# Kernel optimization log

Measured on AMD Instinct MI355X. Metric: run time of the kernel, lower is better.

Reference implementation:

```python
import jax, jax.numpy as jnp
import numpy as np

B, S, D = 16, 16, 4096
H, KV, HD = 32, 8, 128
MAX_B, MAX_S = 16, 4096
START = 4080


def setup_inputs() -> dict:
    key = jax.random.key(0)
    ks = jax.random.split(key, 10)
    sc = 0.02
    # RoPE angles for positions [START, START+S)
    inv_freq = 1.0 / (10000.0 ** (np.arange(0, HD, 2, dtype=np.float32) / HD))  # [HD/2]
    pos = np.arange(START, START + S, dtype=np.float32)
    ang = np.outer(pos, inv_freq)  # [S, HD/2]
    return {
        'x': jax.random.normal(ks[0], (B, S, D), jnp.float32),
        'k': jax.random.normal(ks[1], (B, S, D), jnp.float32),
        'v': jax.random.normal(ks[2], (B, S, D), jnp.float32),
        'wq': jax.random.normal(ks[3], (D, H * HD), jnp.float32) * sc,
        'wk': jax.random.normal(ks[4], (D, KV * HD), jnp.float32) * sc,
        'wv': jax.random.normal(ks[5], (D, KV * HD), jnp.float32) * sc,
        'wo': jax.random.normal(ks[6], (H * HD, D), jnp.float32) * sc,
        'cache_k': jax.random.normal(ks[7], (MAX_B, MAX_S, KV, HD), jnp.float32),
        'cache_v': jax.random.normal(ks[8], (MAX_B, MAX_S, KV, HD), jnp.float32),
        'freqs_cos': jnp.asarray(np.cos(ang)),
        'freqs_sin': jnp.asarray(np.sin(ang)),
        'start_pos': START,
    }


def _rope(t, cos, sin):
    # t: [B,S,nh,HD]; interleaved complex pairs (even=real, odd=imag)
    t2 = t.reshape(*t.shape[:-1], HD // 2, 2)
    x0, x1 = t2[..., 0], t2[..., 1]
    c = cos[None, :, None, :]
    s = sin[None, :, None, :]
    r0 = x0 * c - x1 * s
    r1 = x0 * s + x1 * c
    return jnp.stack([r0, r1], axis=-1).reshape(t.shape)


def reference(x, k, v, wq, wk, wv, wo, cache_k, cache_v, freqs_cos, freqs_sin, start_pos):
    rep = H // KV
    xq = (x @ wq).reshape(B, S, H, HD)
    xk = (k @ wk).reshape(B, S, KV, HD)
    xv = (v @ wv).reshape(B, S, KV, HD)
    xq = _rope(xq, freqs_cos, freqs_sin)
    xk = _rope(xk, freqs_cos, freqs_sin)
    # KV-cache append (start_pos is a static Python int)
    cache_k = jax.lax.dynamic_update_slice(cache_k, xk, (0, start_pos, 0, 0))
    cache_v = jax.lax.dynamic_update_slice(cache_v, xv, (0, start_pos, 0, 0))
    T = start_pos + S
    keys = cache_k[:B, :T]    # [B,T,KV,HD]
    values = cache_v[:B, :T]  # [B,T,KV,HD]
    # GQA without materializing repeat_kv: q head h = g*rep + r
    q = xq.reshape(B, S, KV, rep, HD)
    scores = jnp.einsum('bsgrd,btgd->bgrst', q, keys) / jnp.sqrt(jnp.float32(HD))
    attn = jax.nn.softmax(scores.astype(jnp.float32), axis=-1).astype(q.dtype)
    out = jnp.einsum('bgrst,btgd->bsgrd', attn, values).reshape(B, S, H * HD)
    return out @ wo
```

## Files before the change

kernel.cpp:

```cpp
#include <hip/hip_runtime.h>

typedef __attribute__((ext_vector_type(8))) short bf8_t;
typedef __attribute__((ext_vector_type(4))) short s4_t;
typedef __attribute__((ext_vector_type(4))) float f4_t;

#define DEV static __device__ __forceinline__

DEV short f2bf(float f) {
  union { float f; unsigned u; } x; x.f = f;
  unsigned r = x.u + 0x7FFFu + ((x.u >> 16) & 1u);
  return (short)(r >> 16);
}
DEV float bf2f(short h) {
  union { unsigned u; float f; } x; x.u = ((unsigned)(unsigned short)h) << 16;
  return x.f;
}
DEV f4_t mfma16(bf8_t a, bf8_t b, f4_t c) {
  return __builtin_amdgcn_mfma_f32_16x16x32_bf16(a, b, c, 0, 0, 0);
}
DEV f4_t zf4() { f4_t v = {0.f, 0.f, 0.f, 0.f}; return v; }

DEV void cvt8(const f4_t& f0, const f4_t& f1, bf8_t& hv, bf8_t& lv) {
#pragma unroll
  for (int i = 0; i < 4; i++) {
    short h = f2bf(f0[i]); hv[i] = h; lv[i] = f2bf(f0[i] - bf2f(h));
  }
#pragma unroll
  for (int i = 0; i < 4; i++) {
    short h = f2bf(f1[i]); hv[4 + i] = h; lv[4 + i] = f2bf(f1[i] - bf2f(h));
  }
}

__global__ __launch_bounds__(256, 4)
void qkv_kernel(const float* __restrict__ x, const float* __restrict__ kin,
                const float* __restrict__ vin, const float* __restrict__ wq,
                const float* __restrict__ wk, const float* __restrict__ wv,
                float* __restrict__ part)
{
  __shared__ short Bh[2][64][40], Bl[2][64][40];

  int bid = blockIdx.x;
  int sw = (bid & 7) * 192 + (bid >> 3);
  int ks = sw / 384;
  int r  = sw % 384;

  int lin, N, cbase;
  const float* A; const float* W;
  if (r < 256)      { lin = r;       A = x;   W = wq; N = 4096; cbase = 0; }
  else if (r < 320) { lin = r - 256; A = kin; W = wk; N = 1024; cbase = 4096; }
  else              { lin = r - 320; A = vin; W = wv; N = 1024; cbase = 5120; }
  int m0 = (lin & 3) * 64;
  int n0 = (lin >> 2) * 64;
  int k0 = ks * 1024;

  int tid = threadIdx.x, w = tid >> 6, l = tid & 63;
  f4_t acc[4];
#pragma unroll
  for (int i = 0; i < 4; i++) acc[i] = zf4();

  int bn = tid & 63;
  int bch = (tid >> 6) ^ ((tid >> 3) & 3);
  int bk = bch * 8;
  const float* wptr = W + n0 + bn;

  const float* afrag = A + (m0 + w * 16 + (l & 15)) * 4096 + k0 + (l >> 4) * 8;

  f4_t a0 = *(const f4_t*)afrag;
  f4_t a1 = *(const f4_t*)(afrag + 4);
  float br[8];
#pragma unroll
  for (int j = 0; j < 8; j++) br[j] = wptr[(size_t)(k0 + bk + j) * N];

  for (int it = 0; it < 32; ++it) {
    int cur = it & 1;
    {
      f4_t f0, f1;
#pragma unroll
      for (int j = 0; j < 4; j++) { f0[j] = br[j]; f1[j] = br[4 + j]; }
      bf8_t hv, lv; cvt8(f0, f1, hv, lv);
      *(bf8_t*)&Bh[cur][bn][bk] = hv;
      *(bf8_t*)&Bl[cur][bn][bk] = lv;
    }
    f4_t a0c = a0, a1c = a1;
    if (it + 1 < 32) {
      a0 = *(const f4_t*)(afrag + (it + 1) * 32);
      a1 = *(const f4_t*)(afrag + (it + 1) * 32 + 4);
#pragma unroll
      for (int j = 0; j < 8; j++)
        br[j] = wptr[(size_t)(k0 + (it + 1) * 32 + bk + j) * N];
    }
    __syncthreads();
    bf8_t ah, al; cvt8(a0c, a1c, ah, al);
    __builtin_amdgcn_s_setprio(1);
#pragma unroll
    for (int nt = 0; nt < 4; ++nt) {
      bf8_t bh = *(const bf8_t*)&Bh[cur][nt * 16 + (l & 15)][(l >> 4) * 8];
      bf8_t bl = *(const bf8_t*)&Bl[cur][nt * 16 + (l & 15)][(l >> 4) * 8];
      acc[nt] = mfma16(ah, bh, acc[nt]);
      acc[nt] = mfma16(ah, bl, acc[nt]);
      acc[nt] = mfma16(al, bh, acc[nt]);
    }
    __builtin_amdgcn_s_setprio(0);
  }

  float* po = part + ((size_t)ks * 256 + m0) * 6144 + cbase + n0;
  int cl = l & 15, gq = l >> 4;
#pragma unroll
  for (int nt = 0; nt < 4; ++nt)
#pragma unroll
    for (int i = 0; i < 4; i++)
      po[(w * 16 + gq * 4 + i) * 6144 + nt * 16 + cl] = acc[nt][i];
}

__global__ __launch_bounds__(256)
void reduce_rope(const float* __restrict__ part,
                 const float* __restrict__ fcos, const float* __restrict__ fsin,
                 short* __restrict__ qh, short* __restrict__ ql,
                 short* __restrict__ kh, short* __restrict__ kl,
                 short* __restrict__ vb)
{
  int gid = blockIdx.x * 256 + threadIdx.x;
  int row = gid / 768;
  int c8  = (gid - row * 768) * 8;
  const float* p = part + (size_t)row * 6144 + c8;
  float v[8];
#pragma unroll
  for (int j = 0; j < 8; j++) v[j] = p[j];
#pragma unroll
  for (int ksp = 1; ksp < 4; ksp++) {
    const float* q = p + (size_t)ksp * 256 * 6144;
#pragma unroll
    for (int j = 0; j < 8; j++) v[j] += q[j];
  }
  int s = row & 15, bb = row >> 4;
  if (c8 < 4096) {
    int h = c8 >> 7, d = c8 & 127;
    f4_t c  = *(const f4_t*)(fcos + s * 64 + (d >> 1));
    f4_t sn = *(const f4_t*)(fsin + s * 64 + (d >> 1));
    bf8_t hv, lv;
#pragma unroll
    for (int pr = 0; pr < 4; pr++) {
      float x0 = v[2 * pr], x1 = v[2 * pr + 1];
      float r0 = (x0 * c[pr] - x1 * sn[pr]) * 0.08838834764831845f;
      float r1 = (x0 * sn[pr] + x1 * c[pr]) * 0.08838834764831845f;
      short h0 = f2bf(r0); hv[2 * pr] = h0; lv[2 * pr] = f2bf(r0 - bf2f(h0));
      short h1 = f2bf(r1); hv[2 * pr + 1] = h1; lv[2 * pr + 1] = f2bf(r1 - bf2f(h1));
    }
    int idx = ((bb * 8 + (h >> 2)) * 64 + (h & 3) * 16 + s) * 128 + d;
    *(bf8_t*)(qh + idx) = hv;
    *(bf8_t*)(ql + idx) = lv;
  } else if (c8 < 5120) {
    int cc = c8 - 4096; int h = cc >> 7, d = cc & 127;
    f4_t c  = *(const f4_t*)(fcos + s * 64 + (d >> 1));
    f4_t sn = *(const f4_t*)(fsin + s * 64 + (d >> 1));
    bf8_t hv, lv;
#pragma unroll
    for (int pr = 0; pr < 4; pr++) {
      float x0 = v[2 * pr], x1 = v[2 * pr + 1];
      float r0 = x0 * c[pr] - x1 * sn[pr];
      float r1 = x0 * sn[pr] + x1 * c[pr];
      short h0 = f2bf(r0); hv[2 * pr] = h0; lv[2 * pr] = f2bf(r0 - bf2f(h0));
      short h1 = f2bf(r1); hv[2 * pr + 1] = h1; lv[2 * pr + 1] = f2bf(r1 - bf2f(h1));
    }
    int idx = ((bb * 8 + h) * 16 + s) * 128 + d;
    *(bf8_t*)(kh + idx) = hv;
    *(bf8_t*)(kl + idx) = lv;
  } else {
    int cc = c8 - 5120; int h = cc >> 7, d = cc & 127;
    bf8_t hv;
#pragma unroll
    for (int j = 0; j < 8; j++) hv[j] = f2bf(v[j]);
    int idx = ((bb * 8 + h) * 16 + s) * 128 + d;
    *(bf8_t*)(vb + idx) = hv;
  }
}

__global__ __launch_bounds__(256)
void attn_kernel(const float* __restrict__ ck, const float* __restrict__ cv,
                 const short* __restrict__ qhp, const short* __restrict__ qlp,
                 const short* __restrict__ khp, const short* __restrict__ klp,
                 const short* __restrict__ vbp, const int* __restrict__ startp,
                 float* __restrict__ Op, float* __restrict__ mp,
                 float* __restrict__ lp)
{
  __shared__ short Kh[64][136], Kl[64][136];
  __shared__ short Vt[128][72];
  __shared__ short Ps[4][16][72];

  int bid = blockIdx.x;
  int bg = bid >> 2, sp = bid & 3;
  int b = bg >> 3, g = bg & 7;
  int tid = threadIdx.x, w = tid >> 6, l = tid & 63;
  int start = *startp;

  bf8_t qfh[4], qfl[4];
  {
    int qoff = (bg * 64 + w * 16 + (l & 15)) * 128 + (l >> 4) * 8;
#pragma unroll
    for (int kt = 0; kt < 4; ++kt) {
      qfh[kt] = *(const bf8_t*)(qhp + qoff + kt * 32);
      qfl[kt] = *(const bf8_t*)(qlp + qoff + kt * 32);
    }
  }
  f4_t of[8];
#pragma unroll
  for (int i = 0; i < 8; i++) of[i] = zf4();
  float mrun[4], lrun[4];
#pragma unroll
  for (int i = 0; i < 4; i++) { mrun[i] = -1e30f; lrun[i] = 0.f; }

  int srow = tid >> 2, sdc = (tid & 3) * 32;

  for (int tile = 0; tile < 16; ++tile) {
    int tb = sp * 1024 + tile * 64;
    __syncthreads();
    {
      int t = tb + srow;
      if (t >= start) {
        const short* sh = khp + ((bg * 16) + (t - start)) * 128 + sdc;
        const short* sl = klp + ((bg * 16) + (t - start)) * 128 + sdc;
#pragma unroll
        for (int j = 0; j < 4; j++) {
          *(bf8_t*)&Kh[srow][sdc + j * 8] = *(const bf8_t*)(sh + j * 8);
          *(bf8_t*)&Kl[srow][sdc + j * 8] = *(const bf8_t*)(sl + j * 8);
        }
      } else {
        const float* src = ck + (((size_t)b * 4096 + t) * 8 + g) * 128 + sdc;
#pragma unroll
        for (int j = 0; j < 4; j++) {
          f4_t f0 = *(const f4_t*)(src + j * 8);
          f4_t f1 = *(const f4_t*)(src + j * 8 + 4);
          bf8_t hv, lv; cvt8(f0, f1, hv, lv);
          *(bf8_t*)&Kh[srow][sdc + j * 8] = hv;
          *(bf8_t*)&Kl[srow][sdc + j * 8] = lv;
        }
      }
    }
    {
      int t = tb + srow;
      if (t >= start) {
        const short* sv = vbp + ((bg * 16) + (t - start)) * 128 + sdc;
#pragma unroll
        for (int j = 0; j < 4; j++) {
          bf8_t vv = *(const bf8_t*)(sv + j * 8);
#pragma unroll
          for (int i = 0; i < 8; i++) Vt[sdc + j * 8 + i][srow] = vv[i];
        }
      } else {
        const float* src = cv + (((size_t)b * 4096 + t) * 8 + g) * 128 + sdc;
#pragma unroll
        for (int j = 0; j < 8; j++) {
          f4_t f = *(const f4_t*)(src + j * 4);
#pragma unroll
          for (int i = 0; i < 4; i++) Vt[sdc + j * 4 + i][srow] = f2bf(f[i]);
        }
      }
    }
    __syncthreads();

    f4_t sf[4];
#pragma unroll
    for (int i = 0; i < 4; i++) sf[i] = zf4();
    __builtin_amdgcn_s_setprio(1);
#pragma unroll
    for (int tt = 0; tt < 4; ++tt) {
#pragma unroll
      for (int kt = 0; kt < 4; ++kt) {
        bf8_t kbh = *(const bf8_t*)&Kh[tt * 16 + (l & 15)][kt * 32 + (l >> 4) * 8];
        bf8_t kbl = *(const bf8_t*)&Kl[tt * 16 + (l & 15)][kt * 32 + (l >> 4) * 8];
        sf[tt] = mfma16(qfh[kt], kbh, sf[tt]);
        sf[tt] = mfma16(qfh[kt], kbl, sf[tt]);
        sf[tt] = mfma16(qfl[kt], kbh, sf[tt]);
      }
    }
    __builtin_amdgcn_s_setprio(0);

    float mt[4];
#pragma unroll
    for (int i = 0; i < 4; i++)
      mt[i] = fmaxf(fmaxf(sf[0][i], sf[1][i]), fmaxf(sf[2][i], sf[3][i]));
#pragma unroll
    for (int st = 1; st < 16; st <<= 1)
#pragma unroll
      for (int i = 0; i < 4; i++) mt[i] = fmaxf(mt[i], __shfl_xor(mt[i], st));
    float sc[4];
#pragma unroll
    for (int i = 0; i < 4; i++) {
      float mn = fmaxf(mrun[i], mt[i]);
      sc[i] = __expf(mrun[i] - mn);
      mrun[i] = mn;
    }
    float rs[4] = {0.f, 0.f, 0.f, 0.f};
#pragma unroll
    for (int tt = 0; tt < 4; ++tt)
#pragma unroll
      for (int i = 0; i < 4; i++) {
        float pexp = __expf(sf[tt][i] - mrun[i]);
        rs[i] += pexp;
        Ps[w][(l >> 4) * 4 + i][tt * 16 + (l & 15)] = f2bf(pexp);
      }
#pragma unroll
    for (int st = 1; st < 16; st <<= 1)
#pragma unroll
      for (int i = 0; i < 4; i++) rs[i] += __shfl_xor(rs[i], st);
#pragma unroll
    for (int i = 0; i < 4; i++) lrun[i] = lrun[i] * sc[i] + rs[i];
#pragma unroll
    for (int dt = 0; dt < 8; ++dt)
#pragma unroll
      for (int i = 0; i < 4; i++) of[dt][i] *= sc[i];

    __builtin_amdgcn_s_setprio(1);
#pragma unroll
    for (int kt2 = 0; kt2 < 2; ++kt2) {
      bf8_t pa = *(const bf8_t*)&Ps[w][l & 15][kt2 * 32 + (l >> 4) * 8];
#pragma unroll
      for (int dt = 0; dt < 8; ++dt) {
        bf8_t vf = *(const bf8_t*)&Vt[dt * 16 + (l & 15)][kt2 * 32 + (l >> 4) * 8];
        of[dt] = mfma16(pa, vf, of[dt]);
      }
    }
    __builtin_amdgcn_s_setprio(0);
  }

  size_t obase = ((size_t)(bg * 4 + sp) * 64 + w * 16) * 128;
#pragma unroll
  for (int dt = 0; dt < 8; ++dt)
#pragma unroll
    for (int i = 0; i < 4; i++)
      Op[obase + ((l >> 4) * 4 + i) * 128 + dt * 16 + (l & 15)] = of[dt][i];
  if ((l & 15) == 0) {
    int rbase = (bg * 4 + sp) * 64 + w * 16 + (l >> 4) * 4;
#pragma unroll
    for (int i = 0; i < 4; i++) { mp[rbase + i] = mrun[i]; lp[rbase + i] = lrun[i]; }
  }
}

__global__ __launch_bounds__(256)
void merge_kernel(const float* __restrict__ Op, const float* __restrict__ mp,
                  const float* __restrict__ lp, short* __restrict__ attnb)
{
  int bg = blockIdx.x;
  int tid = threadIdx.x;
  int row = tid >> 2, dc = (tid & 3) * 32;
  int b = bg >> 3, g = bg & 7;
  int r = row >> 4, s = row & 15;
  float mm[4], ww[4];
  float M = -1e30f;
#pragma unroll
  for (int spp = 0; spp < 4; ++spp) {
    mm[spp] = mp[(bg * 4 + spp) * 64 + row];
    M = fmaxf(M, mm[spp]);
  }
  float denom = 0.f;
#pragma unroll
  for (int spp = 0; spp < 4; ++spp) {
    ww[spp] = __expf(mm[spp] - M);
    denom += lp[(bg * 4 + spp) * 64 + row] * ww[spp];
  }
  float inv = 1.0f / denom;
  int ob = (b * 16 + s) * 4096 + (g * 4 + r) * 128 + dc;
#pragma unroll
  for (int j = 0; j < 8; j++) {
    f4_t a = zf4();
#pragma unroll
    for (int spp = 0; spp < 4; ++spp) {
      f4_t o = *(const f4_t*)(Op + ((size_t)(bg * 4 + spp) * 64 + row) * 128 + dc + j * 4);
#pragma unroll
      for (int i = 0; i < 4; i++) a[i] += ww[spp] * o[i];
    }
    s4_t o4;
#pragma unroll
    for (int i = 0; i < 4; i++) o4[i] = f2bf(a[i] * inv);
    *(s4_t*)(attnb + ob + j * 4) = o4;
  }
}

__global__ __launch_bounds__(256, 4)
void wo_kernel(const short* __restrict__ attnb, const float* __restrict__ wo,
               float* __restrict__ wpart)
{
  __shared__ short Bs[2][64][40];

  int bid = blockIdx.x;
  int sw = (bid & 7) * 128 + (bid >> 3);
  int ks = sw >> 8, r = sw & 255;
  int m0 = (r & 3) * 64, n0 = (r >> 2) * 64, k0 = ks * 1024;

  int tid = threadIdx.x, w = tid >> 6, l = tid & 63;
  f4_t acc[4];
#pragma unroll
  for (int i = 0; i < 4; i++) acc[i] = zf4();

  int bn = tid & 63;
  int bch = (tid >> 6) ^ ((tid >> 3) & 3);
  int bk = bch * 8;
  const float* wptr = wo + n0 + bn;
  const short* afrag = attnb + (m0 + w * 16 + (l & 15)) * 4096 + k0 + (l >> 4) * 8;

  bf8_t areg = *(const bf8_t*)afrag;
  float br[8];
#pragma unroll
  for (int j = 0; j < 8; j++) br[j] = wptr[(size_t)(k0 + bk + j) * 4096];

  for (int it = 0; it < 32; ++it) {
    int cur = it & 1;
    {
      bf8_t hv;
#pragma unroll
      for (int j = 0; j < 8; j++) hv[j] = f2bf(br[j]);
      *(bf8_t*)&Bs[cur][bn][bk] = hv;
    }
    bf8_t ac = areg;
    if (it + 1 < 32) {
      areg = *(const bf8_t*)(afrag + (it + 1) * 32);
#pragma unroll
      for (int j = 0; j < 8; j++)
        br[j] = wptr[(size_t)(k0 + (it + 1) * 32 + bk + j) * 4096];
    }
    __syncthreads();
    __builtin_amdgcn_s_setprio(1);
#pragma unroll
    for (int nt = 0; nt < 4; ++nt) {
      bf8_t bb_ = *(const bf8_t*)&Bs[cur][nt * 16 + (l & 15)][(l >> 4) * 8];
      acc[nt] = mfma16(ac, bb_, acc[nt]);
    }
    __builtin_amdgcn_s_setprio(0);
  }

  float* po = wpart + ((size_t)ks * 256 + m0) * 4096 + n0;
  int cl = l & 15, gq = l >> 4;
#pragma unroll
  for (int nt = 0; nt < 4; ++nt)
#pragma unroll
    for (int i = 0; i < 4; i++)
      po[(w * 16 + gq * 4 + i) * 4096 + nt * 16 + cl] = acc[nt][i];
}

__global__ __launch_bounds__(256)
void reduce_out(const float* __restrict__ wpart, float* __restrict__ out)
{
  int gid = blockIdx.x * 256 + threadIdx.x;
  size_t idx4 = (size_t)gid * 4;
  f4_t s = *(const f4_t*)(wpart + idx4);
#pragma unroll
  for (int ksp = 1; ksp < 4; ksp++) {
    f4_t t = *(const f4_t*)(wpart + (size_t)ksp * 1048576 + idx4);
#pragma unroll
    for (int i = 0; i < 4; i++) s[i] += t[i];
  }
  *(f4_t*)(out + idx4) = s;
}

extern "C" void kernel_launch(void* const* d_in, const int* in_sizes, int n_in,
                              void* d_out, int out_size, void* d_ws, size_t ws_size,
                              hipStream_t stream)
{
  const float* x  = (const float*)d_in[0];
  const float* k  = (const float*)d_in[1];
  const float* v  = (const float*)d_in[2];
  const float* wq = (const float*)d_in[3];
  const float* wk = (const float*)d_in[4];
  const float* wv = (const float*)d_in[5];
  const float* wo = (const float*)d_in[6];
  const float* ck = (const float*)d_in[7];
  const float* cv = (const float*)d_in[8];
  const float* fc = (const float*)d_in[9];
  const float* fs = (const float*)d_in[10];
  const int*   spv = (const int*)d_in[11];
  float* out = (float*)d_out;

  char* p = (char*)d_ws;
  float* S = (float*)p; p += (size_t)4 * 256 * 6144 * 4;
  float* qpart = S;
  float* Oppp  = S;
  float* wpart = S;
  short* qh = (short*)p; p += (size_t)128 * 64 * 128 * 2;
  short* ql = (short*)p; p += (size_t)128 * 64 * 128 * 2;
  short* kh = (short*)p; p += (size_t)128 * 16 * 128 * 2;
  short* kl = (short*)p; p += (size_t)128 * 16 * 128 * 2;
  short* vb = (short*)p; p += (size_t)128 * 16 * 128 * 2;
  short* attnb = (short*)p; p += (size_t)256 * 4096 * 2;
  float* mp = (float*)p; p += (size_t)512 * 64 * 4;
  float* lp = (float*)p; p += (size_t)512 * 64 * 4;

  hipLaunchKernelGGL(qkv_kernel, dim3(1536), dim3(256), 0, stream,
                     x, k, v, wq, wk, wv, qpart);
  hipLaunchKernelGGL(reduce_rope, dim3(768), dim3(256), 0, stream,
                     qpart, fc, fs, qh, ql, kh, kl, vb);
  hipLaunchKernelGGL(attn_kernel, dim3(512), dim3(256), 0, stream,
                     ck, cv, qh, ql, kh, kl, vb, spv, Oppp, mp, lp);
  hipLaunchKernelGGL(merge_kernel, dim3(128), dim3(256), 0, stream,
                     Oppp, mp, lp, attnb);
  hipLaunchKernelGGL(wo_kernel, dim3(1024), dim3(256), 0, stream,
                     attnb, wo, wpart);
  hipLaunchKernelGGL(reduce_out, dim3(1024), dim3(256), 0, stream,
                     wpart, out);
}
```

Before: 288.6 us.

## Split attention KV range into 8 chunks with 32-row tiles and coalesced V transpose

Doubles the split-KV factor from 4 to 8 (1024 blocks) and halves the tile size to 32 rows, shrinking shared memory and adding a 5-blocks-per-SM launch bound so more blocks can be resident on the 256 CUs. The V tile load is rewritten so each thread reads one column element across consecutive rows and packs pairs into the transposed layout, instead of doing scattered 16-bit transposed LDS writes. The merge kernel and workspace sizes grow to handle 8 partials. This costs more partial-output traffic and merge work, and adds more sync points per token, in exchange for better occupancy and memory parallelism in the cache-bound attention step.

```diff
diff --git a/kernel.cpp b/kernel.cpp
--- a/kernel.cpp
+++ b/kernel.cpp
@@ -175,7 +175,7 @@
   }
 }
 
-__global__ __launch_bounds__(256)
+__global__ __launch_bounds__(256, 5)
 void attn_kernel(const float* __restrict__ ck, const float* __restrict__ cv,
                  const short* __restrict__ qhp, const short* __restrict__ qlp,
                  const short* __restrict__ khp, const short* __restrict__ klp,
@@ -183,12 +183,12 @@
                  float* __restrict__ Op, float* __restrict__ mp,
                  float* __restrict__ lp)
 {
-  __shared__ short Kh[64][136], Kl[64][136];
-  __shared__ short Vt[128][72];
-  __shared__ short Ps[4][16][72];
+  __shared__ short Kh[32][136], Kl[32][136];
+  __shared__ short Vt[128][40];
+  __shared__ short Ps[4][16][40];
 
   int bid = blockIdx.x;
-  int bg = bid >> 2, sp = bid & 3;
+  int bg = bid >> 3, sp = bid & 7;
   int b = bg >> 3, g = bg & 7;
   int tid = threadIdx.x, w = tid >> 6, l = tid & 63;
   int start = *startp;
@@ -209,61 +209,60 @@
 #pragma unroll
   for (int i = 0; i < 4; i++) { mrun[i] = -1e30f; lrun[i] = 0.f; }
 
-  int srow = tid >> 2, sdc = (tid & 3) * 32;
+  int srow = tid >> 3, sdc = (tid & 7) * 16;
+  int vd = tid & 127, vtg = (tid >> 7) * 16;
 
   for (int tile = 0; tile < 16; ++tile) {
-    int tb = sp * 1024 + tile * 64;
+    int tb = sp * 512 + tile * 32;
     __syncthreads();
     {
       int t = tb + srow;
       if (t >= start) {
         const short* sh = khp + ((bg * 16) + (t - start)) * 128 + sdc;
         const short* sl = klp + ((bg * 16) + (t - start)) * 128 + sdc;
-#pragma unroll
-        for (int j = 0; j < 4; j++) {
-          *(bf8_t*)&Kh[srow][sdc + j * 8] = *(const bf8_t*)(sh + j * 8);
-          *(bf8_t*)&Kl[srow][sdc + j * 8] = *(const bf8_t*)(sl + j * 8);
-        }
+        *(bf8_t*)&Kh[srow][sdc]     = *(const bf8_t*)sh;
+        *(bf8_t*)&Kh[srow][sdc + 8] = *(const bf8_t*)(sh + 8);
+        *(bf8_t*)&Kl[srow][sdc]     = *(const bf8_t*)sl;
+        *(bf8_t*)&Kl[srow][sdc + 8] = *(const bf8_t*)(sl + 8);
       } else {
         const float* src = ck + (((size_t)b * 4096 + t) * 8 + g) * 128 + sdc;
-#pragma unroll
-        for (int j = 0; j < 4; j++) {
-          f4_t f0 = *(const f4_t*)(src + j * 8);
-          f4_t f1 = *(const f4_t*)(src + j * 8 + 4);
-          bf8_t hv, lv; cvt8(f0, f1, hv, lv);
-          *(bf8_t*)&Kh[srow][sdc + j * 8] = hv;
-          *(bf8_t*)&Kl[srow][sdc + j * 8] = lv;
-        }
+        f4_t f0 = *(const f4_t*)src;
+        f4_t f1 = *(const f4_t*)(src + 4);
+        f4_t f2 = *(const f4_t*)(src + 8);
+        f4_t f3 = *(const f4_t*)(src + 12);
+        bf8_t hv, lv;
+        cvt8(f0, f1, hv, lv);
+        *(bf8_t*)&Kh[srow][sdc] = hv;
+        *(bf8_t*)&Kl[srow][sdc] = lv;
+        cvt8(f2, f3, hv, lv);
+        *(bf8_t*)&Kh[srow][sdc + 8] = hv;
+        *(bf8_t*)&Kl[srow][sdc + 8] = lv;
       }
     }
     {
-      int t = tb + srow;
-      if (t >= start) {
-        const short* sv = vbp + ((bg * 16) + (t - start)) * 128 + sdc;
-#pragma unroll
-        for (int j = 0; j < 4; j++) {
-          bf8_t vv = *(const bf8_t*)(sv + j * 8);
-#pragma unroll
-          for (int i = 0; i < 8; i++) Vt[sdc + j * 8 + i][srow] = vv[i];
-        }
-      } else {
-        const float* src = cv + (((size_t)b * 4096 + t) * 8 + g) * 128 + sdc;
-#pragma unroll
-        for (int j = 0; j < 8; j++) {
-          f4_t f = *(const f4_t*)(src + j * 4);
-#pragma unroll
-          for (int i = 0; i < 4; i++) Vt[sdc + j * 4 + i][srow] = f2bf(f[i]);
-        }
+      const float* vsrc = cv + (((size_t)b * 4096) * 8 + g) * 128 + vd;
+      const short* vbs  = vbp + (bg * 16) * 128 + vd;
+#pragma unroll
+      for (int tp = 0; tp < 8; ++tp) {
+        int t0 = tb + vtg + tp * 2;
+        short e0, e1;
+        if (t0 >= start)     e0 = vbs[(t0 - start) * 128];
+        else                 e0 = f2bf(vsrc[(size_t)t0 * 1024]);
+        if (t0 + 1 >= start) e1 = vbs[(t0 + 1 - start) * 128];
+        else                 e1 = f2bf(vsrc[(size_t)(t0 + 1) * 1024]);
+        unsigned pk = (unsigned)(unsigned short)e0 |
+                      ((unsigned)(unsigned short)e1 << 16);
+        *(unsigned*)&Vt[vd][vtg + tp * 2] = pk;
       }
     }
     __syncthreads();
 
-    f4_t sf[4];
-#pragma unroll
-    for (int i = 0; i < 4; i++) sf[i] = zf4();
+    f4_t sf[2];
+#pragma unroll
+    for (int i = 0; i < 2; i++) sf[i] = zf4();
     __builtin_amdgcn_s_setprio(1);
 #pragma unroll
-    for (int tt = 0; tt < 4; ++tt) {
+    for (int tt = 0; tt < 2; ++tt) {
 #pragma unroll
       for (int kt = 0; kt < 4; ++kt) {
         bf8_t kbh = *(const bf8_t*)&Kh[tt * 16 + (l & 15)][kt * 32 + (l >> 4) * 8];
@@ -277,8 +276,7 @@
 
     float mt[4];
 #pragma unroll
-    for (int i = 0; i < 4; i++)
-      mt[i] = fmaxf(fmaxf(sf[0][i], sf[1][i]), fmaxf(sf[2][i], sf[3][i]));
+    for (int i = 0; i < 4; i++) mt[i] = fmaxf(sf[0][i], sf[1][i]);
 #pragma unroll
     for (int st = 1; st < 16; st <<= 1)
 #pragma unroll
@@ -292,7 +290,7 @@
     }
     float rs[4] = {0.f, 0.f, 0.f, 0.f};
 #pragma unroll
-    for (int tt = 0; tt < 4; ++tt)
+    for (int tt = 0; tt < 2; ++tt)
 #pragma unroll
       for (int i = 0; i < 4; i++) {
         float pexp = __expf(sf[tt][i] - mrun[i]);
@@ -311,26 +309,25 @@
       for (int i = 0; i < 4; i++) of[dt][i] *= sc[i];
 
     __builtin_amdgcn_s_setprio(1);
-#pragma unroll
-    for (int kt2 = 0; kt2 < 2; ++kt2) {
-      bf8_t pa = *(const bf8_t*)&Ps[w][l & 15][kt2 * 32 + (l >> 4) * 8];
+    {
+      bf8_t pa = *(const bf8_t*)&Ps[w][l & 15][(l >> 4) * 8];
 #pragma unroll
       for (int dt = 0; dt < 8; ++dt) {
-        bf8_t vf = *(const bf8_t*)&Vt[dt * 16 + (l & 15)][kt2 * 32 + (l >> 4) * 8];
+        bf8_t vf = *(const bf8_t*)&Vt[dt * 16 + (l & 15)][(l >> 4) * 8];
         of[dt] = mfma16(pa, vf, of[dt]);
       }
     }
     __builtin_amdgcn_s_setprio(0);
   }
 
-  size_t obase = ((size_t)(bg * 4 + sp) * 64 + w * 16) * 128;
+  size_t obase = ((size_t)(bg * 8 + sp) * 64 + w * 16) * 128;
 #pragma unroll
   for (int dt = 0; dt < 8; ++dt)
 #pragma unroll
     for (int i = 0; i < 4; i++)
       Op[obase + ((l >> 4) * 4 + i) * 128 + dt * 16 + (l & 15)] = of[dt][i];
   if ((l & 15) == 0) {
-    int rbase = (bg * 4 + sp) * 64 + w * 16 + (l >> 4) * 4;
+    int rbase = (bg * 8 + sp) * 64 + w * 16 + (l >> 4) * 4;
 #pragma unroll
     for (int i = 0; i < 4; i++) { mp[rbase + i] = mrun[i]; lp[rbase + i] = lrun[i]; }
   }
@@ -345,18 +342,18 @@
   int row = tid >> 2, dc = (tid & 3) * 32;
   int b = bg >> 3, g = bg & 7;
   int r = row >> 4, s = row & 15;
-  float mm[4], ww[4];
+  float mm[8], ww[8];
   float M = -1e30f;
 #pragma unroll
-  for (int spp = 0; spp < 4; ++spp) {
-    mm[spp] = mp[(bg * 4 + spp) * 64 + row];
+  for (int spp = 0; spp < 8; ++spp) {
+    mm[spp] = mp[(bg * 8 + spp) * 64 + row];
     M = fmaxf(M, mm[spp]);
   }
   float denom = 0.f;
 #pragma unroll
-  for (int spp = 0; spp < 4; ++spp) {
+  for (int spp = 0; spp < 8; ++spp) {
     ww[spp] = __expf(mm[spp] - M);
-    denom += lp[(bg * 4 + spp) * 64 + row] * ww[spp];
+    denom += lp[(bg * 8 + spp) * 64 + row] * ww[spp];
   }
   float inv = 1.0f / denom;
   int ob = (b * 16 + s) * 4096 + (g * 4 + r) * 128 + dc;
@@ -364,8 +361,8 @@
   for (int j = 0; j < 8; j++) {
     f4_t a = zf4();
 #pragma unroll
-    for (int spp = 0; spp < 4; ++spp) {
-      f4_t o = *(const f4_t*)(Op + ((size_t)(bg * 4 + spp) * 64 + row) * 128 + dc + j * 4);
+    for (int spp = 0; spp < 8; ++spp) {
+      f4_t o = *(const f4_t*)(Op + ((size_t)(bg * 8 + spp) * 64 + row) * 128 + dc + j * 4);
 #pragma unroll
       for (int i = 0; i < 4; i++) a[i] += ww[spp] * o[i];
     }
@@ -471,7 +468,7 @@
   float* out = (float*)d_out;
 
   char* p = (char*)d_ws;
-  float* S = (float*)p; p += (size_t)4 * 256 * 6144 * 4;
+  float* S = (float*)p; p += (size_t)34 * 1024 * 1024;
   float* qpart = S;
   float* Oppp  = S;
   float* wpart = S;
@@ -481,14 +478,14 @@
   short* kl = (short*)p; p += (size_t)128 * 16 * 128 * 2;
   short* vb = (short*)p; p += (size_t)128 * 16 * 128 * 2;
   short* attnb = (short*)p; p += (size_t)256 * 4096 * 2;
-  float* mp = (float*)p; p += (size_t)512 * 64 * 4;
-  float* lp = (float*)p; p += (size_t)512 * 64 * 4;
+  float* mp = (float*)p; p += (size_t)1024 * 64 * 4;
+  float* lp = (float*)p; p += (size_t)1024 * 64 * 4;
 
   hipLaunchKernelGGL(qkv_kernel, dim3(1536), dim3(256), 0, stream,
                      x, k, v, wq, wk, wv, qpart);
   hipLaunchKernelGGL(reduce_rope, dim3(768), dim3(256), 0, stream,
                      qpart, fc, fs, qh, ql, kh, kl, vb);
-  hipLaunchKernelGGL(attn_kernel, dim3(512), dim3(256), 0, stream,
+  hipLaunchKernelGGL(attn_kernel, dim3(1024), dim3(256), 0, stream,
                      ck, cv, qh, ql, kh, kl, vb, spv, Oppp, mp, lp);
   hipLaunchKernelGGL(merge_kernel, dim3(128), dim3(256), 0, stream,
                      Oppp, mp, lp, attnb);
```

Result: slower. 481.2 us (+66.7%).

## Split attention over 8 KV chunks, drop K low-part, store V row-major

Applied to the files above, without the earlier changes.

Attention is split into 8 sequence chunks per batch-group instead of 4, doubling the grid to 1024 blocks, and the merge kernel now combines 8 partials. The K cache is stored only as a bf16 high part, so the score step needs two MFMAs per k-tile instead of three and one fewer LDS buffer. V is written to LDS row-major with packed 32-bit stores, replacing the per-element transposed scatter, and the PV step gathers the B fragment element by element. Launch bounds request 3 blocks per SU. Dropping the K low part reduces score precision, and the strided V gather may cause LDS bank conflicts.

```diff
diff --git a/kernel.cpp b/kernel.cpp
--- a/kernel.cpp
+++ b/kernel.cpp
@@ -116,8 +116,7 @@
 void reduce_rope(const float* __restrict__ part,
                  const float* __restrict__ fcos, const float* __restrict__ fsin,
                  short* __restrict__ qh, short* __restrict__ ql,
-                 short* __restrict__ kh, short* __restrict__ kl,
-                 short* __restrict__ vb)
+                 short* __restrict__ kh, short* __restrict__ vb)
 {
   int gid = blockIdx.x * 256 + threadIdx.x;
   int row = gid / 768;
@@ -153,18 +152,17 @@
     int cc = c8 - 4096; int h = cc >> 7, d = cc & 127;
     f4_t c  = *(const f4_t*)(fcos + s * 64 + (d >> 1));
     f4_t sn = *(const f4_t*)(fsin + s * 64 + (d >> 1));
-    bf8_t hv, lv;
+    bf8_t hv;
 #pragma unroll
     for (int pr = 0; pr < 4; pr++) {
       float x0 = v[2 * pr], x1 = v[2 * pr + 1];
       float r0 = x0 * c[pr] - x1 * sn[pr];
       float r1 = x0 * sn[pr] + x1 * c[pr];
-      short h0 = f2bf(r0); hv[2 * pr] = h0; lv[2 * pr] = f2bf(r0 - bf2f(h0));
-      short h1 = f2bf(r1); hv[2 * pr + 1] = h1; lv[2 * pr + 1] = f2bf(r1 - bf2f(h1));
+      hv[2 * pr]     = f2bf(r0);
+      hv[2 * pr + 1] = f2bf(r1);
     }
     int idx = ((bb * 8 + h) * 16 + s) * 128 + d;
     *(bf8_t*)(kh + idx) = hv;
-    *(bf8_t*)(kl + idx) = lv;
   } else {
     int cc = c8 - 5120; int h = cc >> 7, d = cc & 127;
     bf8_t hv;
@@ -175,20 +173,20 @@
   }
 }
 
-__global__ __launch_bounds__(256)
+__global__ __launch_bounds__(256, 3)
 void attn_kernel(const float* __restrict__ ck, const float* __restrict__ cv,
                  const short* __restrict__ qhp, const short* __restrict__ qlp,
-                 const short* __restrict__ khp, const short* __restrict__ klp,
-                 const short* __restrict__ vbp, const int* __restrict__ startp,
+                 const short* __restrict__ khp, const short* __restrict__ vbp,
+                 const int* __restrict__ startp,
                  float* __restrict__ Op, float* __restrict__ mp,
                  float* __restrict__ lp)
 {
-  __shared__ short Kh[64][136], Kl[64][136];
-  __shared__ short Vt[128][72];
+  __shared__ short Kh[64][136];
+  __shared__ short Vs[64][130];
   __shared__ short Ps[4][16][72];
 
   int bid = blockIdx.x;
-  int bg = bid >> 2, sp = bid & 3;
+  int bg = bid >> 3, sp = bid & 7;
   int b = bg >> 3, g = bg & 7;
   int tid = threadIdx.x, w = tid >> 6, l = tid & 63;
   int start = *startp;
@@ -211,48 +209,54 @@
 
   int srow = tid >> 2, sdc = (tid & 3) * 32;
 
-  for (int tile = 0; tile < 16; ++tile) {
-    int tb = sp * 1024 + tile * 64;
+  for (int tile = 0; tile < 8; ++tile) {
+    int tb = sp * 512 + tile * 64;
+    int t = tb + srow;
     __syncthreads();
     {
-      int t = tb + srow;
       if (t >= start) {
         const short* sh = khp + ((bg * 16) + (t - start)) * 128 + sdc;
-        const short* sl = klp + ((bg * 16) + (t - start)) * 128 + sdc;
-#pragma unroll
-        for (int j = 0; j < 4; j++) {
-          *(bf8_t*)&Kh[srow][sdc + j * 8] = *(const bf8_t*)(sh + j * 8);
-          *(bf8_t*)&Kl[srow][sdc + j * 8] = *(const bf8_t*)(sl + j * 8);
-        }
+#pragma unroll
+        for (int j = 0; j < 4; j++)
+          *(bf8_t*)&Kh[srow][sdc + 8 * j] = *(const bf8_t*)(sh + 8 * j);
       } else {
         const float* src = ck + (((size_t)b * 4096 + t) * 8 + g) * 128 + sdc;
 #pragma unroll
         for (int j = 0; j < 4; j++) {
-          f4_t f0 = *(const f4_t*)(src + j * 8);
-          f4_t f1 = *(const f4_t*)(src + j * 8 + 4);
-          bf8_t hv, lv; cvt8(f0, f1, hv, lv);
-          *(bf8_t*)&Kh[srow][sdc + j * 8] = hv;
-          *(bf8_t*)&Kl[srow][sdc + j * 8] = lv;
+          f4_t f0 = *(const f4_t*)(src + 8 * j);
+          f4_t f1 = *(const f4_t*)(src + 8 * j + 4);
+          bf8_t hv;
+#pragma unroll
+          for (int i = 0; i < 4; i++) { hv[i] = f2bf(f0[i]); hv[4 + i] = f2bf(f1[i]); }
+          *(bf8_t*)&Kh[srow][sdc + 8 * j] = hv;
         }
       }
     }
     {
-      int t = tb + srow;
+      unsigned* vdst = (unsigned*)&Vs[srow][sdc];
       if (t >= start) {
         const short* sv = vbp + ((bg * 16) + (t - start)) * 128 + sdc;
 #pragma unroll
         for (int j = 0; j < 4; j++) {
-          bf8_t vv = *(const bf8_t*)(sv + j * 8);
-#pragma unroll
-          for (int i = 0; i < 8; i++) Vt[sdc + j * 8 + i][srow] = vv[i];
+          bf8_t vv = *(const bf8_t*)(sv + 8 * j);
+          union { bf8_t v; unsigned u[4]; } cu; cu.v = vv;
+#pragma unroll
+          for (int q = 0; q < 4; q++) vdst[4 * j + q] = cu.u[q];
         }
       } else {
         const float* src = cv + (((size_t)b * 4096 + t) * 8 + g) * 128 + sdc;
 #pragma unroll
-        for (int j = 0; j < 8; j++) {
-          f4_t f = *(const f4_t*)(src + j * 4);
-#pragma unroll
-          for (int i = 0; i < 4; i++) Vt[sdc + j * 4 + i][srow] = f2bf(f[i]);
+        for (int j = 0; j < 4; j++) {
+          f4_t f0 = *(const f4_t*)(src + 8 * j);
+          f4_t f1 = *(const f4_t*)(src + 8 * j + 4);
+#pragma unroll
+          for (int q = 0; q < 2; q++)
+            vdst[4 * j + q] = (unsigned)(unsigned short)f2bf(f0[2 * q]) |
+                              ((unsigned)(unsigned short)f2bf(f0[2 * q + 1]) << 16);
+#pragma unroll
+          for (int q = 0; q < 2; q++)
+            vdst[4 * j + 2 + q] = (unsigned)(unsigned short)f2bf(f1[2 * q]) |
+                                  ((unsigned)(unsigned short)f2bf(f1[2 * q + 1]) << 16);
         }
       }
     }
@@ -266,11 +270,9 @@
     for (int tt = 0; tt < 4; ++tt) {
 #pragma unroll
       for (int kt = 0; kt < 4; ++kt) {
-        bf8_t kbh = *(const bf8_t*)&Kh[tt * 16 + (l & 15)][kt * 32 + (l >> 4) * 8];
-        bf8_t kbl = *(const bf8_t*)&Kl[tt * 16 + (l & 15)][kt * 32 + (l >> 4) * 8];
-        sf[tt] = mfma16(qfh[kt], kbh, sf[tt]);
-        sf[tt] = mfma16(qfh[kt], kbl, sf[tt]);
-        sf[tt] = mfma16(qfl[kt], kbh, sf[tt]);
+        bf8_t kb = *(const bf8_t*)&Kh[tt * 16 + (l & 15)][kt * 32 + (l >> 4) * 8];
+        sf[tt] = mfma16(qfh[kt], kb, sf[tt]);
+        sf[tt] = mfma16(qfl[kt], kb, sf[tt]);
       }
     }
     __builtin_amdgcn_s_setprio(0);
@@ -314,23 +316,27 @@
 #pragma unroll
     for (int kt2 = 0; kt2 < 2; ++kt2) {
       bf8_t pa = *(const bf8_t*)&Ps[w][l & 15][kt2 * 32 + (l >> 4) * 8];
+      int trow = kt2 * 32 + (l >> 4) * 8;
 #pragma unroll
       for (int dt = 0; dt < 8; ++dt) {
-        bf8_t vf = *(const bf8_t*)&Vt[dt * 16 + (l & 15)][kt2 * 32 + (l >> 4) * 8];
+        int dcol = dt * 16 + (l & 15);
+        bf8_t vf;
+#pragma unroll
+        for (int e = 0; e < 8; ++e) vf[e] = Vs[trow + e][dcol];
         of[dt] = mfma16(pa, vf, of[dt]);
       }
     }
     __builtin_amdgcn_s_setprio(0);
   }
 
-  size_t obase = ((size_t)(bg * 4 + sp) * 64 + w * 16) * 128;
+  size_t obase = ((size_t)(bg * 8 + sp) * 64 + w * 16) * 128;
 #pragma unroll
   for (int dt = 0; dt < 8; ++dt)
 #pragma unroll
     for (int i = 0; i < 4; i++)
       Op[obase + ((l >> 4) * 4 + i) * 128 + dt * 16 + (l & 15)] = of[dt][i];
   if ((l & 15) == 0) {
-    int rbase = (bg * 4 + sp) * 64 + w * 16 + (l >> 4) * 4;
+    int rbase = (bg * 8 + sp) * 64 + w * 16 + (l >> 4) * 4;
 #pragma unroll
     for (int i = 0; i < 4; i++) { mp[rbase + i] = mrun[i]; lp[rbase + i] = lrun[i]; }
   }
@@ -345,18 +351,18 @@
   int row = tid >> 2, dc = (tid & 3) * 32;
   int b = bg >> 3, g = bg & 7;
   int r = row >> 4, s = row & 15;
-  float mm[4], ww[4];
+  float mm[8], ww[8];
   float M = -1e30f;
 #pragma unroll
-  for (int spp = 0; spp < 4; ++spp) {
-    mm[spp] = mp[(bg * 4 + spp) * 64 + row];
+  for (int spp = 0; spp < 8; ++spp) {
+    mm[spp] = mp[(bg * 8 + spp) * 64 + row];
     M = fmaxf(M, mm[spp]);
   }
   float denom = 0.f;
 #pragma unroll
-  for (int spp = 0; spp < 4; ++spp) {
+  for (int spp = 0; spp < 8; ++spp) {
     ww[spp] = __expf(mm[spp] - M);
-    denom += lp[(bg * 4 + spp) * 64 + row] * ww[spp];
+    denom += lp[(bg * 8 + spp) * 64 + row] * ww[spp];
   }
   float inv = 1.0f / denom;
   int ob = (b * 16 + s) * 4096 + (g * 4 + r) * 128 + dc;
@@ -364,8 +370,8 @@
   for (int j = 0; j < 8; j++) {
     f4_t a = zf4();
 #pragma unroll
-    for (int spp = 0; spp < 4; ++spp) {
-      f4_t o = *(const f4_t*)(Op + ((size_t)(bg * 4 + spp) * 64 + row) * 128 + dc + j * 4);
+    for (int spp = 0; spp < 8; ++spp) {
+      f4_t o = *(const f4_t*)(Op + ((size_t)(bg * 8 + spp) * 64 + row) * 128 + dc + j * 4);
 #pragma unroll
       for (int i = 0; i < 4; i++) a[i] += ww[spp] * o[i];
     }
@@ -471,25 +477,24 @@
   float* out = (float*)d_out;
 
   char* p = (char*)d_ws;
-  float* S = (float*)p; p += (size_t)4 * 256 * 6144 * 4;
+  float* S = (float*)p; p += (size_t)34 * 1024 * 1024;
   float* qpart = S;
   float* Oppp  = S;
   float* wpart = S;
   short* qh = (short*)p; p += (size_t)128 * 64 * 128 * 2;
   short* ql = (short*)p; p += (size_t)128 * 64 * 128 * 2;
   short* kh = (short*)p; p += (size_t)128 * 16 * 128 * 2;
-  short* kl = (short*)p; p += (size_t)128 * 16 * 128 * 2;
   short* vb = (short*)p; p += (size_t)128 * 16 * 128 * 2;
   short* attnb = (short*)p; p += (size_t)256 * 4096 * 2;
-  float* mp = (float*)p; p += (size_t)512 * 64 * 4;
-  float* lp = (float*)p; p += (size_t)512 * 64 * 4;
+  float* mp = (float*)p; p += (size_t)1024 * 64 * 4;
+  float* lp = (float*)p; p += (size_t)1024 * 64 * 4;
 
   hipLaunchKernelGGL(qkv_kernel, dim3(1536), dim3(256), 0, stream,
                      x, k, v, wq, wk, wv, qpart);
   hipLaunchKernelGGL(reduce_rope, dim3(768), dim3(256), 0, stream,
-                     qpart, fc, fs, qh, ql, kh, kl, vb);
-  hipLaunchKernelGGL(attn_kernel, dim3(512), dim3(256), 0, stream,
-                     ck, cv, qh, ql, kh, kl, vb, spv, Oppp, mp, lp);
+                     qpart, fc, fs, qh, ql, kh, vb);
+  hipLaunchKernelGGL(attn_kernel, dim3(1024), dim3(256), 0, stream,
+                     ck, cv, qh, ql, kh, vb, spv, Oppp, mp, lp);
   hipLaunchKernelGGL(merge_kernel, dim3(128), dim3(256), 0, stream,
                      Oppp, mp, lp, attnb);
   hipLaunchKernelGGL(wo_kernel, dim3(1024), dim3(256), 0, stream,
```

After: 293.4 us. No clear change (+1.7%).
